# Kernel optimization log

Hardware: AMD Instinct MI355X
Metric: run time of the kernel (lower is better)

The kernel has to match this reference:

```python
import jax, jax.numpy as jnp
import numpy as np

B, C, D, H, W = 2, 128, 16, 96, 96


def setup_inputs() -> dict:
    key = jax.random.key(0)
    k1, k2 = jax.random.split(key)
    x = jax.random.normal(k1, (B, C, D, H, W), dtype=jnp.float32)
    gamma = jax.random.uniform(k2, (1,), dtype=jnp.float32)
    return {"x": x, "gamma": gamma}


def reference(x, gamma):
    b, c, d, h, w = x.shape
    n = d * h * w
    q = x.reshape(b, c, n)                      # [B,C,N] query==key==value
    # energy: [B,C,C] = q @ q^T
    energy = jnp.einsum('bcn,bdn->bcd', q, q)
    # EnergyMaxNorm: rowwise max (AdaptiveMaxPool1d(1) over last dim) minus energy
    e_max = jnp.max(energy, axis=-1, keepdims=True)
    energy = e_max - energy
    attn = jax.nn.softmax(energy, axis=-1)      # [B,C,C]
    out = jnp.einsum('bcd,bdn->bcn', attn, q)   # [B,C,N]
    out = out.reshape(b, c, d, h, w)
    # gamma-scaled residual fusion (modulation_type 'addition')
    return x + gamma[0] * out
```

## Files before the change

### kernel.cpp

```cpp
#include <hip/hip_runtime.h>

typedef unsigned short u16;
typedef unsigned int u32;
typedef __attribute__((ext_vector_type(8))) short short8;
typedef __attribute__((ext_vector_type(4))) float f32x4;
typedef __attribute__((ext_vector_type(4))) u16 u16x4;

#define NBATCH 2
#define NC 128
#define NN 147456
#define NCHUNK 1152
#define G1_PARTS 256
#define N3_PER_B 1152

__device__ __forceinline__ u16 bf16rne(float f) {
  u32 u = __builtin_bit_cast(u32, f);
  return (u16)((u + 0x7FFFu + ((u >> 16) & 1u)) >> 16);
}
__device__ __forceinline__ float bf2f(u16 h) {
  u32 u = ((u32)h) << 16;
  return __builtin_bit_cast(float, u);
}

__global__ __launch_bounds__(256, 2)
void gram_k(const float* __restrict__ x, float* __restrict__ part) {
  __shared__ u16 hi[128 * 128];
  __shared__ u16 lo[128 * 128];
  const int tid = threadIdx.x;
  const int bid = blockIdx.x;
  const int b   = bid >> 8;
  const int pi  = bid & 255;
  const int w   = tid >> 6;
  const int l   = tid & 63;
  const int grp = l >> 4;
  const int lr  = l & 15;
  const int swz = lr << 3;
  const float* xb = x + (size_t)b * NC * NN;

  f32x4 acc[2][8];
#pragma unroll
  for (int i = 0; i < 2; ++i)
#pragma unroll
    for (int j = 0; j < 8; ++j) acc[i][j] = (f32x4){0.f, 0.f, 0.f, 0.f};

  const int lrow = tid >> 5;
  const int lcol = (tid & 31) << 2;

  for (int ch = pi; ch < NCHUNK; ch += G1_PARTS) {
    const int k0 = ch << 7;
    __syncthreads();
#pragma unroll
    for (int j = 0; j < 16; ++j) {
      const int row = (j << 3) + lrow;
      const float4 v = *(const float4*)(xb + (size_t)row * NN + (k0 + lcol));
      const u16 h0 = bf16rne(v.x), h1 = bf16rne(v.y), h2 = bf16rne(v.z), h3 = bf16rne(v.w);
      const u16 g0 = bf16rne(v.x - bf2f(h0)), g1 = bf16rne(v.y - bf2f(h1));
      const u16 g2 = bf16rne(v.z - bf2f(h2)), g3 = bf16rne(v.w - bf2f(h3));
      const int idx = (row << 7) + (lcol ^ ((row & 15) << 3));
      *(u16x4*)(hi + idx) = (u16x4){h0, h1, h2, h3};
      *(u16x4*)(lo + idx) = (u16x4){g0, g1, g2, g3};
    }
    __syncthreads();

    const int m0 = (w << 5) + lr;
    const int m1 = m0 + 16;
#pragma unroll
    for (int kk = 0; kk < 128; kk += 32) {
      const int kb = kk + (grp << 3);
      const short8 Ah0 = *(const short8*)(hi + (m0 << 7) + (kb ^ swz));
      const short8 Al0 = *(const short8*)(lo + (m0 << 7) + (kb ^ swz));
      const short8 Ah1 = *(const short8*)(hi + (m1 << 7) + (kb ^ swz));
      const short8 Al1 = *(const short8*)(lo + (m1 << 7) + (kb ^ swz));
#pragma unroll
      for (int nt = 0; nt < 8; ++nt) {
        const int nr  = (nt << 4) + lr;
        const int bix = (nr << 7) + (kb ^ swz);
        const short8 Bh = *(const short8*)(hi + bix);
        const short8 Bl = *(const short8*)(lo + bix);
        acc[0][nt] = __builtin_amdgcn_mfma_f32_16x16x32_bf16(Ah0, Bh, acc[0][nt], 0, 0, 0);
        acc[0][nt] = __builtin_amdgcn_mfma_f32_16x16x32_bf16(Ah0, Bl, acc[0][nt], 0, 0, 0);
        acc[0][nt] = __builtin_amdgcn_mfma_f32_16x16x32_bf16(Al0, Bh, acc[0][nt], 0, 0, 0);
        acc[1][nt] = __builtin_amdgcn_mfma_f32_16x16x32_bf16(Ah1, Bh, acc[1][nt], 0, 0, 0);
        acc[1][nt] = __builtin_amdgcn_mfma_f32_16x16x32_bf16(Ah1, Bl, acc[1][nt], 0, 0, 0);
        acc[1][nt] = __builtin_amdgcn_mfma_f32_16x16x32_bf16(Al1, Bh, acc[1][nt], 0, 0, 0);
      }
    }
  }

  float* pb = part + (size_t)bid * 16384;
#pragma unroll
  for (int mt = 0; mt < 2; ++mt)
#pragma unroll
    for (int nt = 0; nt < 8; ++nt)
#pragma unroll
      for (int r = 0; r < 4; ++r) {
        const int row = (w << 5) + (mt << 4) + (grp << 2) + r;
        const int col = (nt << 4) + lr;
        pb[(row << 7) + col] = acc[mt][nt][r];
      }
}

__global__ __launch_bounds__(128)
void soft_k(const float* __restrict__ part, u16* __restrict__ attn) {
  const int b = blockIdx.x >> 7;
  const int c = blockIdx.x & 127;
  const int d = threadIdx.x;
  __shared__ float red[128];
  float e = 0.f;
  const float* p0 = part + ((size_t)(b * G1_PARTS) << 14) + (c << 7) + d;
  for (int p = 0; p < G1_PARTS; ++p) e += p0[(size_t)p << 14];
  red[d] = e;
  __syncthreads();
#pragma unroll
  for (int s = 64; s > 0; s >>= 1) {
    if (d < s) red[d] = fminf(red[d], red[d + s]);
    __syncthreads();
  }
  const float emin = red[0];
  __syncthreads();
  const float pr = __expf(emin - e);
  red[d] = pr;
  __syncthreads();
#pragma unroll
  for (int s = 64; s > 0; s >>= 1) {
    if (d < s) red[d] += red[d + s];
    __syncthreads();
  }
  const float inv = 1.f / red[0];
  attn[(((size_t)b) << 14) + (c << 7) + d] = bf16rne(pr * inv);
}

__global__ __launch_bounds__(256, 2)
void pv_k(const float* __restrict__ x, const u16* __restrict__ attn,
          const float* __restrict__ gamma, float* __restrict__ out) {
  __shared__ u16 at[128 * 128];
  const int tid = threadIdx.x;
  const int bid = blockIdx.x;
  const int b   = bid / N3_PER_B;
  const int nb  = (bid % N3_PER_B) << 7;
  const int w   = tid >> 6, l = tid & 63, grp = l >> 4, lr = l & 15;
  const int swz = lr << 3;
  const size_t bbase = (size_t)b * NC * NN;
  const u16* ab = attn + (((size_t)b) << 14);

#pragma unroll
  for (int j = 0; j < 8; ++j) {
    const int idx = (j << 8) + tid;
    const int c  = idx >> 4;
    const int d0 = (idx & 15) << 3;
    const int dst = (c << 7) + (d0 ^ ((c & 15) << 3));
    *(short8*)(at + dst) = *(const short8*)(ab + (c << 7) + d0);
  }
  __syncthreads();

  f32x4 acc[8][2];
#pragma unroll
  for (int i = 0; i < 8; ++i) {
    acc[i][0] = (f32x4){0.f, 0.f, 0.f, 0.f};
    acc[i][1] = (f32x4){0.f, 0.f, 0.f, 0.f};
  }

  const int n0 = nb + (w << 5) + lr;
#pragma unroll
  for (int kk = 0; kk < 128; kk += 32) {
    const int d0 = kk + (grp << 3);
    short8 Bh[2], Bl[2];
#pragma unroll
    for (int t = 0; t < 2; ++t) {
      const int n = n0 + (t << 4);
      const float* src = x + bbase + (size_t)d0 * NN + n;
      float f[8];
#pragma unroll
      for (int i = 0; i < 8; ++i) f[i] = src[(size_t)i * NN];
      u16 h[8], g[8];
#pragma unroll
      for (int i = 0; i < 8; ++i) {
        h[i] = bf16rne(f[i]);
        g[i] = bf16rne(f[i] - bf2f(h[i]));
      }
      Bh[t] = (short8){(short)h[0], (short)h[1], (short)h[2], (short)h[3],
                       (short)h[4], (short)h[5], (short)h[6], (short)h[7]};
      Bl[t] = (short8){(short)g[0], (short)g[1], (short)g[2], (short)g[3],
                       (short)g[4], (short)g[5], (short)g[6], (short)g[7]};
    }
#pragma unroll
    for (int mt = 0; mt < 8; ++mt) {
      const int mrow = (mt << 4) + lr;
      const short8 Ah = *(const short8*)(at + (mrow << 7) + ((kk + (grp << 3)) ^ swz));
#pragma unroll
      for (int t = 0; t < 2; ++t) {
        acc[mt][t] = __builtin_amdgcn_mfma_f32_16x16x32_bf16(Ah, Bh[t], acc[mt][t], 0, 0, 0);
        acc[mt][t] = __builtin_amdgcn_mfma_f32_16x16x32_bf16(Ah, Bl[t], acc[mt][t], 0, 0, 0);
      }
    }
  }

  const float gm = gamma[0];
#pragma unroll
  for (int mt = 0; mt < 8; ++mt)
#pragma unroll
    for (int t = 0; t < 2; ++t)
#pragma unroll
      for (int r = 0; r < 4; ++r) {
        const int c = (mt << 4) + (grp << 2) + r;
        const int n = n0 + (t << 4);
        const size_t off = bbase + (size_t)c * NN + n;
        out[off] = x[off] + gm * acc[mt][t][r];
      }
}

extern "C" void kernel_launch(void* const* d_in, const int* in_sizes, int n_in,
                              void* d_out, int out_size, void* d_ws, size_t ws_size,
                              hipStream_t stream) {
  (void)in_sizes; (void)n_in; (void)out_size; (void)ws_size;
  const float* x     = (const float*)d_in[0];
  const float* gamma = (const float*)d_in[1];
  float* out  = (float*)d_out;
  u16*   attn = (u16*)d_ws;
  float* part = out;

  gram_k<<<dim3(2 * G1_PARTS), dim3(256), 0, stream>>>(x, part);
  soft_k<<<dim3(2 * 128),      dim3(128), 0, stream>>>(part, attn);
  pv_k  <<<dim3(2 * N3_PER_B), dim3(256), 0, stream>>>(x, attn, gamma, out);
}
```

Measured before the change: 140.4 us.

## Double-buffer gram kernel LDS with register prefetch of next chunk

The gram kernel now processes 64-column chunks and uses two LDS buffers for the hi/lo bf16 splits. Global loads for the next chunk are issued into registers before the MFMA work on the current chunk, then staged into the other buffer, so there is one barrier per iteration and load latency overlaps compute. The hi part is now made by truncating instead of round-to-nearest, which makes the split cheaper while the lo residual still captures the error. The cost is more registers for the prefetched float4 values, plus twice as many loop iterations with a narrower K per barrier.

```diff
diff --git a/kernel.cpp b/kernel.cpp
--- a/kernel.cpp
+++ b/kernel.cpp
@@ -9,7 +9,8 @@
 #define NBATCH 2
 #define NC 128
 #define NN 147456
-#define NCHUNK 1152
+#define CH 64
+#define NCH (NN / CH)
 #define G1_PARTS 256
 #define N3_PER_B 1152
 
@@ -21,11 +22,17 @@
   u32 u = ((u32)h) << 16;
   return __builtin_bit_cast(float, u);
 }
+__device__ __forceinline__ void split2(float f, u16& h, u16& g) {
+  u32 u = __builtin_bit_cast(u32, f);
+  h = (u16)(u >> 16);
+  float hf = __builtin_bit_cast(float, u & 0xFFFF0000u);
+  g = bf16rne(f - hf);
+}
 
 __global__ __launch_bounds__(256, 2)
 void gram_k(const float* __restrict__ x, float* __restrict__ part) {
-  __shared__ u16 hi[128 * 128];
-  __shared__ u16 lo[128 * 128];
+  __shared__ u16 hi[2][128 * CH];
+  __shared__ u16 lo[2][128 * CH];
   const int tid = threadIdx.x;
   const int bid = blockIdx.x;
   const int b   = bid >> 8;
@@ -34,49 +41,58 @@
   const int l   = tid & 63;
   const int grp = l >> 4;
   const int lr  = l & 15;
-  const int swz = lr << 3;
+  const int swz = (lr & 7) << 3;
   const float* xb = x + (size_t)b * NC * NN;
 
+  const int col4 = tid & 15;
+  const int r0   = tid >> 4;
+
   f32x4 acc[2][8];
 #pragma unroll
   for (int i = 0; i < 2; ++i)
 #pragma unroll
     for (int j = 0; j < 8; ++j) acc[i][j] = (f32x4){0.f, 0.f, 0.f, 0.f};
 
-  const int lrow = tid >> 5;
-  const int lcol = (tid & 31) << 2;
-
-  for (int ch = pi; ch < NCHUNK; ch += G1_PARTS) {
-    const int k0 = ch << 7;
-    __syncthreads();
-#pragma unroll
-    for (int j = 0; j < 16; ++j) {
-      const int row = (j << 3) + lrow;
-      const float4 v = *(const float4*)(xb + (size_t)row * NN + (k0 + lcol));
-      const u16 h0 = bf16rne(v.x), h1 = bf16rne(v.y), h2 = bf16rne(v.z), h3 = bf16rne(v.w);
-      const u16 g0 = bf16rne(v.x - bf2f(h0)), g1 = bf16rne(v.y - bf2f(h1));
-      const u16 g2 = bf16rne(v.z - bf2f(h2)), g3 = bf16rne(v.w - bf2f(h3));
-      const int idx = (row << 7) + (lcol ^ ((row & 15) << 3));
-      *(u16x4*)(hi + idx) = (u16x4){h0, h1, h2, h3};
-      *(u16x4*)(lo + idx) = (u16x4){g0, g1, g2, g3};
-    }
-    __syncthreads();
-
-    const int m0 = (w << 5) + lr;
-    const int m1 = m0 + 16;
-#pragma unroll
-    for (int kk = 0; kk < 128; kk += 32) {
-      const int kb = kk + (grp << 3);
-      const short8 Ah0 = *(const short8*)(hi + (m0 << 7) + (kb ^ swz));
-      const short8 Al0 = *(const short8*)(lo + (m0 << 7) + (kb ^ swz));
-      const short8 Ah1 = *(const short8*)(hi + (m1 << 7) + (kb ^ swz));
-      const short8 Al1 = *(const short8*)(lo + (m1 << 7) + (kb ^ swz));
+  float4 v[8];
+
+  auto issue = [&](int ch) {
+    const int k0 = ch * CH + (col4 << 2);
+#pragma unroll
+    for (int j = 0; j < 8; ++j)
+      v[j] = *(const float4*)(xb + (size_t)(r0 + (j << 4)) * NN + k0);
+  };
+  auto stage = [&](int bb) {
+    u16* H = &hi[bb][0];
+    u16* L = &lo[bb][0];
+#pragma unroll
+    for (int j = 0; j < 8; ++j) {
+      const int row = r0 + (j << 4);
+      const int idx = (row << 6) + ((col4 << 2) ^ ((row & 7) << 3));
+      u16 h0, h1, h2, h3, g0, g1, g2, g3;
+      split2(v[j].x, h0, g0); split2(v[j].y, h1, g1);
+      split2(v[j].z, h2, g2); split2(v[j].w, h3, g3);
+      *(u16x4*)(H + idx) = (u16x4){h0, h1, h2, h3};
+      *(u16x4*)(L + idx) = (u16x4){g0, g1, g2, g3};
+    }
+  };
+  const int m0 = (w << 5) + lr;
+  const int m1 = m0 + 16;
+  auto mma = [&](int bb) {
+    const u16* H = &hi[bb][0];
+    const u16* L = &lo[bb][0];
+#pragma unroll
+    for (int kk = 0; kk < CH; kk += 32) {
+      const int kv = (kk + (grp << 3)) ^ swz;
+      const short8 Ah0 = *(const short8*)(H + (m0 << 6) + kv);
+      const short8 Al0 = *(const short8*)(L + (m0 << 6) + kv);
+      const short8 Ah1 = *(const short8*)(H + (m1 << 6) + kv);
+      const short8 Al1 = *(const short8*)(L + (m1 << 6) + kv);
 #pragma unroll
       for (int nt = 0; nt < 8; ++nt) {
         const int nr  = (nt << 4) + lr;
-        const int bix = (nr << 7) + (kb ^ swz);
-        const short8 Bh = *(const short8*)(hi + bix);
-        const short8 Bl = *(const short8*)(lo + bix);
+        const int bix = (nr << 6) + kv;
+        const short8 Bh = *(const short8*)(H + bix);
+        const short8 Bl = *(const short8*)(L + bix);
         acc[0][nt] = __builtin_amdgcn_mfma_f32_16x16x32_bf16(Ah0, Bh, acc[0][nt], 0, 0, 0);
         acc[0][nt] = __builtin_amdgcn_mfma_f32_16x16x32_bf16(Ah0, Bl, acc[0][nt], 0, 0, 0);
         acc[0][nt] = __builtin_amdgcn_mfma_f32_16x16x32_bf16(Al0, Bh, acc[0][nt], 0, 0, 0);
@@ -85,6 +101,18 @@
         acc[1][nt] = __builtin_amdgcn_mfma_f32_16x16x32_bf16(Al1, Bh, acc[1][nt], 0, 0, 0);
       }
     }
+  };
+
+  issue(pi);
+  stage(0);
+  __syncthreads();
+
+  const int NITER = NCH / G1_PARTS;
+  for (int i = 0; i < NITER; ++i) {
+    if (i + 1 < NITER) issue(pi + (i + 1) * G1_PARTS);
+    mma(i & 1);
+    if (i + 1 < NITER) stage((i + 1) & 1);
+    __syncthreads();
   }
 
   float* pb = part + (size_t)bid * 16384;
```

Result: faster. 118.5 us (-15.6%).
